# Optimization experiments

Hardware: AMD Instinct MI355X
Metric: run time of the kernel (lower is better)

## Reference

```python
import jax, jax.numpy as jnp
import numpy as np


def setup_inputs() -> dict:
    key = jax.random.key(0)
    k1, k2 = jax.random.split(key)
    B, C, H, W = 32, 64, 64, 64
    K = 512
    z_e = jax.random.normal(k1, (B, C, H, W), dtype=jnp.float32)
    # codebook initialized uniform(-1/K, 1/K) as in the torch module
    codebook = jax.random.uniform(k2, (K, C), dtype=jnp.float32,
                                  minval=-1.0 / K, maxval=1.0 / K)
    return {"z_e": z_e, "codebook": codebook}


def reference(z_e, codebook):
    B, C, H, W = z_e.shape
    commitment_cost = 0.25
    # [B*H*W, C]
    z_flat = jnp.transpose(z_e, (0, 2, 3, 1)).reshape(-1, C)
    dists = (jnp.sum(z_flat * z_flat, axis=1, keepdims=True)
             + jnp.sum(codebook * codebook, axis=1)
             - 2.0 * jnp.matmul(z_flat, codebook.T))
    encoding_indices = jnp.argmin(dists, axis=1)  # [N] int
    z_q = codebook[encoding_indices].reshape(B, H, W, C)
    z_q = jnp.transpose(z_q, (0, 3, 1, 2))  # [B, C, H, W]
    q_loss = jnp.mean((z_q - jax.lax.stop_gradient(z_e)) ** 2)
    e_loss = jnp.mean((z_e - jax.lax.stop_gradient(z_q)) ** 2)
    loss = q_loss + commitment_cost * e_loss
    # straight-through estimator
    z_q_st = z_e + jax.lax.stop_gradient(z_q - z_e)
    return (z_q_st, encoding_indices, loss)
```

## Files before the change

kernel.cpp:

```cpp
#include <hip/hip_runtime.h>
#include <cfloat>

typedef __attribute__((ext_vector_type(8))) short short8;
typedef __attribute__((ext_vector_type(4))) float f32x4;

constexpr int C_DIM    = 64;
constexpr int K_CODES  = 512;
constexpr int HW       = 4096;
constexpr int CHW      = 262144;
constexpr int NPTS     = 131072;
constexpr int ZQ_SIZE  = 8388608;
constexpr int IDX_OFF  = ZQ_SIZE;
constexpr int LOSS_OFF = ZQ_SIZE + NPTS;
constexpr int TILE     = 128;
constexpr int EH_STRIDE = 72;
constexpr int CHUNK    = 128;
constexpr int NSLOT    = 16;
constexpr size_t WS_BF16 = (size_t)K_CODES * C_DIM * 2;
constexpr size_t WS_NEED = WS_BF16 + (size_t)K_CODES * 4;

__device__ __forceinline__ unsigned short f32_to_bf16_rne(float f) {
    unsigned u = __float_as_uint(f);
    unsigned r = u + 0x7fffu + ((u >> 16) & 1u);
    return (unsigned short)(r >> 16);
}

template <int STRIDE>
__device__ __forceinline__ float np_sumsq64(const float* __restrict__ a) {
    float r[8];
#pragma unroll
    for (int j = 0; j < 8; ++j) { const float v = a[j * STRIDE]; r[j] = __fmul_rn(v, v); }
#pragma unroll
    for (int i = 8; i < 64; i += 8)
#pragma unroll
        for (int j = 0; j < 8; ++j) {
            const float v = a[(i + j) * STRIDE];
            r[j] = __fadd_rn(r[j], __fmul_rn(v, v));
        }
    return __fadd_rn(
        __fadd_rn(__fadd_rn(r[0], r[1]), __fadd_rn(r[2], r[3])),
        __fadd_rn(__fadd_rn(r[4], r[5]), __fadd_rn(r[6], r[7])));
}

__global__ void vq_zero(float* __restrict__ out) { out[LOSS_OFF] = 0.0f; }

__global__ void vq_prep(const float* __restrict__ cb, unsigned short* __restrict__ wsb,
                        float* __restrict__ wsB, float* __restrict__ out) {
    const int gid = blockIdx.x * 256 + threadIdx.x;
    wsb[gid] = f32_to_bf16_rne(cb[gid]);
    if (gid < K_CODES) wsB[gid] = np_sumsq64<1>(cb + gid * C_DIM);
    if (gid == 0) out[LOSS_OFF] = 0.0f;
}

__global__ __launch_bounds__(256, 4) void vq_idx(const float* __restrict__ ze,
                                                 const float* __restrict__ cb,
                                                 float* __restrict__ out,
                                                 const unsigned short* __restrict__ wsb,
                                                 const float* __restrict__ wsB,
                                                 int use_ws)
{
    __shared__ unsigned short eh[CHUNK * EH_STRIDE];
    __shared__ float  BsL[K_CODES];
    __shared__ float  As[TILE];
    __shared__ unsigned short cand[TILE * NSLOT];
    __shared__ int    cnt[TILE];
    __shared__ int    bestk[TILE];
    __shared__ double lred[4];

    const int tid  = threadIdx.x;
    const int lane = tid & 63, w = tid >> 6;
    const int quad = lane >> 4, l15 = lane & 15;
    const int n0   = blockIdx.x * TILE;
    const int b    = n0 >> 12, hw0 = n0 & (HW - 1);
    const float* zebase = ze + b * CHW + hw0;

    if (use_ws) { for (int k = tid; k < K_CODES; k += 256) BsL[k] = wsB[k]; }
    else        { for (int k = tid; k < K_CODES; k += 256) BsL[k] = np_sumsq64<1>(cb + k * C_DIM); }
    if (tid < TILE) { As[tid] = np_sumsq64<HW>(zebase + tid); cnt[tid] = 0; }
    __syncthreads();

    short8 afr[2][2];
    float  A_pt[2][4], thr[2][4], runmin[2][4];
#pragma unroll
    for (int rt = 0; rt < 2; ++rt) {
        const int pt = w * 32 + rt * 16 + l15;
#pragma unroll
        for (int kc = 0; kc < 2; ++kc) {
            union { unsigned short s[8]; short8 v; } u;
#pragma unroll
            for (int j = 0; j < 8; ++j) {
                const int c = kc * 32 + quad * 8 + j;
                u.s[j] = f32_to_bf16_rne(zebase[c * HW + pt]);
            }
            afr[rt][kc] = u.v;
        }
#pragma unroll
        for (int r = 0; r < 4; ++r) {
            A_pt[rt][r]   = As[w * 32 + rt * 16 + quad * 4 + r];
            runmin[rt][r] = FLT_MAX;
        }
    }

    auto stage = [&](int ch) {
        const int row = tid >> 1, half = tid & 1;
        uint4* dst = (uint4*)(eh + row * EH_STRIDE + half * 32);
        if (use_ws) {
            const uint4* src = (const uint4*)(wsb + (size_t)(ch * CHUNK + row) * C_DIM + half * 32);
#pragma unroll
            for (int i = 0; i < 4; ++i) dst[i] = src[i];
        } else {
            const float4* src = (const float4*)(cb + (size_t)(ch * CHUNK + row) * C_DIM + half * 32);
#pragma unroll
            for (int i = 0; i < 4; ++i) {
                const float4 f0 = src[2 * i], f1 = src[2 * i + 1];
                uint4 o;
                o.x = (unsigned)f32_to_bf16_rne(f0.x) | ((unsigned)f32_to_bf16_rne(f0.y) << 16);
                o.y = (unsigned)f32_to_bf16_rne(f0.z) | ((unsigned)f32_to_bf16_rne(f0.w) << 16);
                o.z = (unsigned)f32_to_bf16_rne(f1.x) | ((unsigned)f32_to_bf16_rne(f1.y) << 16);
                o.w = (unsigned)f32_to_bf16_rne(f1.z) | ((unsigned)f32_to_bf16_rne(f1.w) << 16);
                dst[i] = o;
            }
        }
    };

    for (int ch = 0; ch < 4; ++ch) {
        __syncthreads(); stage(ch); __syncthreads();
        for (int tile = 0; tile < 8; ++tile) {
            const int cl = tile * 16 + l15;
            const short8 b0 = *(const short8*)(eh + cl * EH_STRIDE + quad * 8);
            const short8 b1 = *(const short8*)(eh + cl * EH_STRIDE + 32 + quad * 8);
            const float bs = BsL[ch * CHUNK + cl];
#pragma unroll
            for (int rt = 0; rt < 2; ++rt) {
                f32x4 acc = {0.f, 0.f, 0.f, 0.f};
                acc = __builtin_amdgcn_mfma_f32_16x16x32_bf16(afr[rt][0], b0, acc, 0, 0, 0);
                acc = __builtin_amdgcn_mfma_f32_16x16x32_bf16(afr[rt][1], b1, acc, 0, 0, 0);
#pragma unroll
                for (int r = 0; r < 4; ++r) {
                    const float D = fmaf(-2.f, acc[r], __fadd_rn(A_pt[rt][r], bs));
                    runmin[rt][r] = fminf(runmin[rt][r], D);
                }
            }
        }
    }
#pragma unroll
    for (int rt = 0; rt < 2; ++rt)
#pragma unroll
        for (int r = 0; r < 4; ++r) {
            float v = runmin[rt][r];
#pragma unroll
            for (int m = 1; m < 16; m <<= 1) v = fminf(v, __shfl_xor(v, m, 64));
            thr[rt][r] = v + (4e-4f * sqrtf(A_pt[rt][r]) + 3e-4f);
        }

    for (int ch = 0; ch < 4; ++ch) {
        __syncthreads(); stage(ch); __syncthreads();
        for (int tile = 0; tile < 8; ++tile) {
            const int cl = tile * 16 + l15;
            const short8 b0 = *(const short8*)(eh + cl * EH_STRIDE + quad * 8);
            const short8 b1 = *(const short8*)(eh + cl * EH_STRIDE + 32 + quad * 8);
            const float bs = BsL[ch * CHUNK + cl];
#pragma unroll
            for (int rt = 0; rt < 2; ++rt) {
                f32x4 acc = {0.f, 0.f, 0.f, 0.f};
                acc = __builtin_amdgcn_mfma_f32_16x16x32_bf16(afr[rt][0], b0, acc, 0, 0, 0);
                acc = __builtin_amdgcn_mfma_f32_16x16x32_bf16(afr[rt][1], b1, acc, 0, 0, 0);
#pragma unroll
                for (int r = 0; r < 4; ++r) {
                    const float D = fmaf(-2.f, acc[r], __fadd_rn(A_pt[rt][r], bs));
                    if (D <= thr[rt][r]) {
                        const int pt = w * 32 + rt * 16 + quad * 4 + r;
                        const int p = atomicAdd(&cnt[pt], 1);
                        if (p < NSLOT) cand[pt * NSLOT + p] = (unsigned short)(ch * CHUNK + cl);
                    }
                }
            }
        }
    }
    __syncthreads();

    if (tid < TILE) {
        const float Av = As[tid];
        const int c = cnt[tid];
        float bD = FLT_MAX; int bK = K_CODES;
        if (c <= NSLOT) {
            for (int i = 0; i < c; ++i) {
                const int k = cand[tid * NSLOT + i];
                const float* er = cb + k * C_DIM;
                float M = 0.f;
#pragma unroll
                for (int cc = 0; cc < 64; ++cc) M = fmaf(zebase[cc * HW + tid], er[cc], M);
                const float D = fmaf(-2.f, M, __fadd_rn(Av, BsL[k]));
                if (D < bD || (D == bD && k < bK)) { bD = D; bK = k; }
            }
        } else {
            for (int k = 0; k < K_CODES; ++k) {
                const float* er = cb + k * C_DIM;
                float M = 0.f;
#pragma unroll
                for (int cc = 0; cc < 64; ++cc) M = fmaf(zebase[cc * HW + tid], er[cc], M);
                const float D = fmaf(-2.f, M, __fadd_rn(Av, BsL[k]));
                if (D < bD) { bD = D; bK = k; }
            }
        }
        bestk[tid] = bK;
        out[IDX_OFF + n0 + tid] = (float)bK;
    }
    __syncthreads();

    double ls = 0.0;
#pragma unroll
    for (int it = 0; it < 8; ++it) {
        const int task = tid + 256 * it;
        const int c = task >> 5, q = task & 31;
        const float4 xz = *(const float4*)(zebase + c * HW + 4 * q);
        float o[4];
#pragma unroll
        for (int j = 0; j < 4; ++j) {
            const int k = bestk[4 * q + j];
            const float ev = cb[k * C_DIM + c];
            const float xv = (j == 0) ? xz.x : (j == 1) ? xz.y : (j == 2) ? xz.z : xz.w;
            const float d = __fsub_rn(ev, xv);
            o[j] = __fadd_rn(xv, d);
            ls = fma((double)d, (double)d, ls);
        }
        *(float4*)(out + b * CHW + c * HW + hw0 + 4 * q) = make_float4(o[0], o[1], o[2], o[3]);
    }
#pragma unroll
    for (int off = 32; off > 0; off >>= 1) ls += __shfl_xor(ls, off, 64);
    if ((tid & 63) == 0) lred[w] = ls;
    __syncthreads();
    if (tid == 0)
        atomicAdd(out + LOSS_OFF,
                  (float)((lred[0] + lred[1] + lred[2] + lred[3]) * (1.25 / (double)ZQ_SIZE)));
}

extern "C" void kernel_launch(void* const* d_in, const int* in_sizes, int n_in,
                              void* d_out, int out_size, void* d_ws, size_t ws_size,
                              hipStream_t stream) {
    (void)in_sizes; (void)n_in; (void)out_size;
    const float* ze = (const float*)d_in[0];
    const float* cb = (const float*)d_in[1];
    float* out = (float*)d_out;
    const int use_ws = (ws_size >= WS_NEED) ? 1 : 0;
    unsigned short* wsb = (unsigned short*)d_ws;
    float* wsB = (float*)((char*)d_ws + WS_BF16);

    if (use_ws) vq_prep<<<(K_CODES * C_DIM) / 256, 256, 0, stream>>>(cb, wsb, wsB, out);
    else        vq_zero<<<1, 1, 0, stream>>>(out);
    vq_idx<<<NPTS / TILE, 256, 0, stream>>>(ze, cb, out, wsb, wsB, use_ws);
}
```

Before: 138.7 us.

## Stage full bf16 codebook in LDS once in MFMA fragment layout, double block size

The bf16 codebook is now pre-swizzled in the prep kernel into the MFMA B-fragment order, and the whole 64 KB codebook is loaded into shared memory once per block. This removes the per-chunk restaging and the barriers in both distance passes. Blocks grow to 512 threads covering 256 points, so each codebook load is reused across twice as many points. The cost is much larger LDS use per block (over 64 KB), which limits occupancy per CU, and the fragment reads drop the padded stride.

```diff
diff --git a/kernel.cpp b/kernel.cpp
--- a/kernel.cpp
+++ b/kernel.cpp
@@ -12,10 +12,10 @@
 constexpr int ZQ_SIZE  = 8388608;
 constexpr int IDX_OFF  = ZQ_SIZE;
 constexpr int LOSS_OFF = ZQ_SIZE + NPTS;
-constexpr int TILE     = 128;
-constexpr int EH_STRIDE = 72;
-constexpr int CHUNK    = 128;
+constexpr int TILE     = 256;
+constexpr int THREADS  = 512;
 constexpr int NSLOT    = 16;
+constexpr int NCHUNK   = 4096;
 constexpr size_t WS_BF16 = (size_t)K_CODES * C_DIM * 2;
 constexpr size_t WS_NEED = WS_BF16 + (size_t)K_CODES * 4;
 
@@ -47,25 +47,28 @@
 __global__ void vq_prep(const float* __restrict__ cb, unsigned short* __restrict__ wsb,
                         float* __restrict__ wsB, float* __restrict__ out) {
     const int gid = blockIdx.x * 256 + threadIdx.x;
-    wsb[gid] = f32_to_bf16_rne(cb[gid]);
+    const int j = gid & 7, i = gid >> 3;
+    const int cl = i & 15, q = (i >> 4) & 3, h = (i >> 6) & 1, t = i >> 7;
+    const int k = t * 16 + cl, c = h * 32 + q * 8 + j;
+    wsb[gid] = f32_to_bf16_rne(cb[k * C_DIM + c]);
     if (gid < K_CODES) wsB[gid] = np_sumsq64<1>(cb + gid * C_DIM);
     if (gid == 0) out[LOSS_OFF] = 0.0f;
 }
 
-__global__ __launch_bounds__(256, 4) void vq_idx(const float* __restrict__ ze,
-                                                 const float* __restrict__ cb,
-                                                 float* __restrict__ out,
-                                                 const unsigned short* __restrict__ wsb,
-                                                 const float* __restrict__ wsB,
-                                                 int use_ws)
+__global__ __launch_bounds__(THREADS, 4) void vq_idx(const float* __restrict__ ze,
+                                                     const float* __restrict__ cb,
+                                                     float* __restrict__ out,
+                                                     const unsigned short* __restrict__ wsb,
+                                                     const float* __restrict__ wsB,
+                                                     int use_ws)
 {
-    __shared__ unsigned short eh[CHUNK * EH_STRIDE];
+    __shared__ uint4  eh4[NCHUNK];
     __shared__ float  BsL[K_CODES];
     __shared__ float  As[TILE];
     __shared__ unsigned short cand[TILE * NSLOT];
     __shared__ int    cnt[TILE];
     __shared__ int    bestk[TILE];
-    __shared__ double lred[4];
+    __shared__ double lred[8];
 
     const int tid  = threadIdx.x;
     const int lane = tid & 63, w = tid >> 6;
@@ -74,8 +77,27 @@
     const int b    = n0 >> 12, hw0 = n0 & (HW - 1);
     const float* zebase = ze + b * CHW + hw0;
 
-    if (use_ws) { for (int k = tid; k < K_CODES; k += 256) BsL[k] = wsB[k]; }
-    else        { for (int k = tid; k < K_CODES; k += 256) BsL[k] = np_sumsq64<1>(cb + k * C_DIM); }
+    if (use_ws) {
+        BsL[tid] = wsB[tid];
+        const uint4* src = (const uint4*)wsb;
+#pragma unroll
+        for (int i = 0; i < 8; ++i) eh4[tid + THREADS * i] = src[tid + THREADS * i];
+    } else {
+        for (int k = tid; k < K_CODES; k += THREADS) BsL[k] = np_sumsq64<1>(cb + k * C_DIM);
+#pragma unroll
+        for (int it = 0; it < 8; ++it) {
+            const int i = tid + THREADS * it;
+            const int cl = i & 15, q = (i >> 4) & 3, h = (i >> 6) & 1, t = i >> 7;
+            const float* src = cb + (t * 16 + cl) * C_DIM + h * 32 + q * 8;
+            const float4 f0 = *(const float4*)src, f1 = *(const float4*)(src + 4);
+            uint4 o;
+            o.x = (unsigned)f32_to_bf16_rne(f0.x) | ((unsigned)f32_to_bf16_rne(f0.y) << 16);
+            o.y = (unsigned)f32_to_bf16_rne(f0.z) | ((unsigned)f32_to_bf16_rne(f0.w) << 16);
+            o.z = (unsigned)f32_to_bf16_rne(f1.x) | ((unsigned)f32_to_bf16_rne(f1.y) << 16);
+            o.w = (unsigned)f32_to_bf16_rne(f1.z) | ((unsigned)f32_to_bf16_rne(f1.w) << 16);
+            eh4[i] = o;
+        }
+    }
     if (tid < TILE) { As[tid] = np_sumsq64<HW>(zebase + tid); cnt[tid] = 0; }
     __syncthreads();
 
@@ -101,45 +123,19 @@
         }
     }
 
-    auto stage = [&](int ch) {
-        const int row = tid >> 1, half = tid & 1;
-        uint4* dst = (uint4*)(eh + row * EH_STRIDE + half * 32);
-        if (use_ws) {
-            const uint4* src = (const uint4*)(wsb + (size_t)(ch * CHUNK + row) * C_DIM + half * 32);
-#pragma unroll
-            for (int i = 0; i < 4; ++i) dst[i] = src[i];
-        } else {
-            const float4* src = (const float4*)(cb + (size_t)(ch * CHUNK + row) * C_DIM + half * 32);
-#pragma unroll
-            for (int i = 0; i < 4; ++i) {
-                const float4 f0 = src[2 * i], f1 = src[2 * i + 1];
-                uint4 o;
-                o.x = (unsigned)f32_to_bf16_rne(f0.x) | ((unsigned)f32_to_bf16_rne(f0.y) << 16);
-                o.y = (unsigned)f32_to_bf16_rne(f0.z) | ((unsigned)f32_to_bf16_rne(f0.w) << 16);
-                o.z = (unsigned)f32_to_bf16_rne(f1.x) | ((unsigned)f32_to_bf16_rne(f1.y) << 16);
-                o.w = (unsigned)f32_to_bf16_rne(f1.z) | ((unsigned)f32_to_bf16_rne(f1.w) << 16);
-                dst[i] = o;
-            }
-        }
-    };
-
-    for (int ch = 0; ch < 4; ++ch) {
-        __syncthreads(); stage(ch); __syncthreads();
-        for (int tile = 0; tile < 8; ++tile) {
-            const int cl = tile * 16 + l15;
-            const short8 b0 = *(const short8*)(eh + cl * EH_STRIDE + quad * 8);
-            const short8 b1 = *(const short8*)(eh + cl * EH_STRIDE + 32 + quad * 8);
-            const float bs = BsL[ch * CHUNK + cl];
-#pragma unroll
-            for (int rt = 0; rt < 2; ++rt) {
-                f32x4 acc = {0.f, 0.f, 0.f, 0.f};
-                acc = __builtin_amdgcn_mfma_f32_16x16x32_bf16(afr[rt][0], b0, acc, 0, 0, 0);
-                acc = __builtin_amdgcn_mfma_f32_16x16x32_bf16(afr[rt][1], b1, acc, 0, 0, 0);
-#pragma unroll
-                for (int r = 0; r < 4; ++r) {
-                    const float D = fmaf(-2.f, acc[r], __fadd_rn(A_pt[rt][r], bs));
-                    runmin[rt][r] = fminf(runmin[rt][r], D);
-                }
+    for (int t = 0; t < 32; ++t) {
+        const short8 b0 = *(const short8*)&eh4[(t * 8 + quad) * 16 + l15];
+        const short8 b1 = *(const short8*)&eh4[(t * 8 + 4 + quad) * 16 + l15];
+        const float  bs = BsL[t * 16 + l15];
+#pragma unroll
+        for (int rt = 0; rt < 2; ++rt) {
+            f32x4 acc = {0.f, 0.f, 0.f, 0.f};
+            acc = __builtin_amdgcn_mfma_f32_16x16x32_bf16(afr[rt][0], b0, acc, 0, 0, 0);
+            acc = __builtin_amdgcn_mfma_f32_16x16x32_bf16(afr[rt][1], b1, acc, 0, 0, 0);
+#pragma unroll
+            for (int r = 0; r < 4; ++r) {
+                const float D = fmaf(-2.f, acc[r], __fadd_rn(A_pt[rt][r], bs));
+                runmin[rt][r] = fminf(runmin[rt][r], D);
             }
         }
     }
@@ -153,26 +149,22 @@
             thr[rt][r] = v + (4e-4f * sqrtf(A_pt[rt][r]) + 3e-4f);
         }
 
-    for (int ch = 0; ch < 4; ++ch) {
-        __syncthreads(); stage(ch); __syncthreads();
-        for (int tile = 0; tile < 8; ++tile) {
-            const int cl = tile * 16 + l15;
-            const short8 b0 = *(const short8*)(eh + cl * EH_STRIDE + quad * 8);
-            const short8 b1 = *(const short8*)(eh + cl * EH_STRIDE + 32 + quad * 8);
-            const float bs = BsL[ch * CHUNK + cl];
-#pragma unroll
-            for (int rt = 0; rt < 2; ++rt) {
-                f32x4 acc = {0.f, 0.f, 0.f, 0.f};
-                acc = __builtin_amdgcn_mfma_f32_16x16x32_bf16(afr[rt][0], b0, acc, 0, 0, 0);
-                acc = __builtin_amdgcn_mfma_f32_16x16x32_bf16(afr[rt][1], b1, acc, 0, 0, 0);
-#pragma unroll
-                for (int r = 0; r < 4; ++r) {
-                    const float D = fmaf(-2.f, acc[r], __fadd_rn(A_pt[rt][r], bs));
-                    if (D <= thr[rt][r]) {
-                        const int pt = w * 32 + rt * 16 + quad * 4 + r;
-                        const int p = atomicAdd(&cnt[pt], 1);
-                        if (p < NSLOT) cand[pt * NSLOT + p] = (unsigned short)(ch * CHUNK + cl);
-                    }
+    for (int t = 0; t < 32; ++t) {
+        const short8 b0 = *(const short8*)&eh4[(t * 8 + quad) * 16 + l15];
+        const short8 b1 = *(const short8*)&eh4[(t * 8 + 4 + quad) * 16 + l15];
+        const float  bs = BsL[t * 16 + l15];
+#pragma unroll
+        for (int rt = 0; rt < 2; ++rt) {
+            f32x4 acc = {0.f, 0.f, 0.f, 0.f};
+            acc = __builtin_amdgcn_mfma_f32_16x16x32_bf16(afr[rt][0], b0, acc, 0, 0, 0);
+            acc = __builtin_amdgcn_mfma_f32_16x16x32_bf16(afr[rt][1], b1, acc, 0, 0, 0);
+#pragma unroll
+            for (int r = 0; r < 4; ++r) {
+                const float D = fmaf(-2.f, acc[r], __fadd_rn(A_pt[rt][r], bs));
+                if (D <= thr[rt][r]) {
+                    const int pt = w * 32 + rt * 16 + quad * 4 + r;
+                    const int p = atomicAdd(&cnt[pt], 1);
+                    if (p < NSLOT) cand[pt * NSLOT + p] = (unsigned short)(t * 16 + l15);
                 }
             }
         }
@@ -211,8 +203,8 @@
     double ls = 0.0;
 #pragma unroll
     for (int it = 0; it < 8; ++it) {
-        const int task = tid + 256 * it;
-        const int c = task >> 5, q = task & 31;
+        const int task = tid + THREADS * it;
+        const int c = task >> 6, q = task & 63;
         const float4 xz = *(const float4*)(zebase + c * HW + 4 * q);
         float o[4];
 #pragma unroll
@@ -230,9 +222,12 @@
     for (int off = 32; off > 0; off >>= 1) ls += __shfl_xor(ls, off, 64);
     if ((tid & 63) == 0) lred[w] = ls;
     __syncthreads();
-    if (tid == 0)
-        atomicAdd(out + LOSS_OFF,
-                  (float)((lred[0] + lred[1] + lred[2] + lred[3]) * (1.25 / (double)ZQ_SIZE)));
+    if (tid == 0) {
+        double t = 0.0;
+#pragma unroll
+        for (int i = 0; i < 8; ++i) t += lred[i];
+        atomicAdd(out + LOSS_OFF, (float)(t * (1.25 / (double)ZQ_SIZE)));
+    }
 }
 
 extern "C" void kernel_launch(void* const* d_in, const int* in_sizes, int n_in,
@@ -248,5 +243,5 @@
 
     if (use_ws) vq_prep<<<(K_CODES * C_DIM) / 256, 256, 0, stream>>>(cb, wsb, wsB, out);
     else        vq_zero<<<1, 1, 0, stream>>>(out);
-    vq_idx<<<NPTS / TILE, 256, 0, stream>>>(ze, cb, out, wsb, wsB, use_ws);
-}
+    vq_idx<<<NPTS / TILE, THREADS, 0, stream>>>(ze, cb, out, wsb, wsB, use_ws);
+}
```

Result: no change. 139.6 us (+0.6%).
